# Performance work log

Measured on AMD Instinct MI355X. Metric: run time of the kernel, lower is better.

## Reference

```python
import jax, jax.numpy as jnp
import numpy as np

N_TOKENS = 100000
CUT = [0, 20000, 50000, 100000]  # cutoff_ends
D = 1024


def setup_inputs() -> dict:
    key = jax.random.key(0)
    ks = jax.random.split(key, 12)
    B, S = 2, 1024
    hidden = jax.random.normal(ks[0], (B, S, D), dtype=jnp.float32)
    target = jax.random.randint(ks[1], (B, S), 0, N_TOKENS, dtype=jnp.int64)
    s = 0.02
    # cluster 0 (shortlist) + cluster projection head
    w0 = jax.random.normal(ks[2], (20000, 1024), dtype=jnp.float32) * s
    b0 = jnp.zeros((20000,), jnp.float32)
    cluster_w = jax.random.normal(ks[3], (2, 1024), dtype=jnp.float32) * s  # n_clusters=2
    cluster_b = jnp.zeros((2,), jnp.float32)
    proj0 = jax.random.normal(ks[4], (1024, 1024), dtype=jnp.float32) * s  # d_proj x d_emb_0
    # tail cluster 1: d_emb_1 = 1024 // 4 = 256, vocab slice 20000..50000
    w1 = jax.random.normal(ks[5], (30000, 256), dtype=jnp.float32) * s
    b1 = jnp.zeros((30000,), jnp.float32)
    proj1 = jax.random.normal(ks[6], (1024, 256), dtype=jnp.float32) * s
    # tail cluster 2: d_emb_2 = 1024 // 16 = 64, vocab slice 50000..100000
    w2 = jax.random.normal(ks[7], (50000, 64), dtype=jnp.float32) * s
    b2 = jnp.zeros((50000,), jnp.float32)
    proj2 = jax.random.normal(ks[8], (1024, 64), dtype=jnp.float32) * s
    return {"hidden": hidden, "target": target,
            "w0": w0, "b0": b0, "cluster_w": cluster_w, "cluster_b": cluster_b, "proj0": proj0,
            "w1": w1, "b1": b1, "proj1": proj1,
            "w2": w2, "b2": b2, "proj2": proj2}


def reference(hidden, target, w0, b0, cluster_w, cluster_b, proj0,
              w1, b1, proj1, w2, b2, proj2):
    tgt_shape = target.shape
    h = hidden.reshape(-1, D)            # [N, d_proj]
    t = target.reshape(-1)               # [N]

    # head: shortlist logits + cluster logits, via low-rank projection
    head_w = jnp.concatenate([w0, cluster_w], axis=0)   # [20002, 1024]
    head_b = jnp.concatenate([b0, cluster_b], axis=0)
    head_logit = (h @ proj0) @ head_w.T + head_b        # [N, 20002]
    head_lp = jax.nn.log_softmax(head_logit, axis=1)

    nll = jnp.zeros(t.shape, h.dtype)

    # cluster 0 (shortlist): logprob is head_lp at the target id
    m0 = t < CUT[1]
    idx0 = jnp.clip(t, 0, CUT[1] - 1)
    lp0 = jnp.take_along_axis(head_lp, idx0[:, None], axis=1)[:, 0]
    nll = jnp.where(m0, -lp0, nll)

    # tail clusters. NOTE: faithful to original quirk head_logprob[:, -i]
    tails = [(CUT[1], CUT[2], w1, b1, proj1), (CUT[2], CUT[3], w2, b2, proj2)]
    for i, (left, right, w, b, p) in enumerate(tails, start=1):
        m = (t >= left) & (t < right)
        tail_logit = (h @ p) @ w.T + b                  # [N, right-left]
        tail_lp = jax.nn.log_softmax(tail_logit, axis=1)
        ti = jnp.clip(t - left, 0, right - left - 1)
        lp = head_lp[:, -i] + jnp.take_along_axis(tail_lp, ti[:, None], axis=1)[:, 0]
        nll = jnp.where(m, -lp, nll)

    return nll.reshape(tgt_shape)
```

## Files before the change

### kernel.cpp

```cpp
#include <hip/hip_runtime.h>
#include <cstdint>
#include <cstddef>

#define DEV static __device__ __forceinline__

typedef __attribute__((ext_vector_type(8))) short bf16x8_t;
typedef __attribute__((ext_vector_type(4))) float f32x4_t;

DEV unsigned short f2bf(float f) {
  union { float f; unsigned u; } v; v.f = f;
  unsigned r = v.u + 0x7fffu + ((v.u >> 16) & 1u);
  return (unsigned short)(r >> 16);
}

DEV void gl_lds16(const void* g, void* l) {
  __builtin_amdgcn_global_load_lds(
      (const __attribute__((address_space(1))) void*)g,
      (__attribute__((address_space(3))) void*)l,
      16, 0, 0);
}

__global__ __launch_bounds__(256)
void prep_k(const int* __restrict__ target,
            int* __restrict__ idx1, int* __restrict__ pos1,
            int* __restrict__ idx2, int* __restrict__ pos2,
            int* __restrict__ cnts,
            const float* __restrict__ p0, const float* __restrict__ p1,
            const float* __restrict__ p2, unsigned short* __restrict__ pAll,
            const float* __restrict__ s0, unsigned short* __restrict__ d0, int n0,
            const float* __restrict__ s1, unsigned short* __restrict__ d1, int n1,
            const float* __restrict__ s2, unsigned short* __restrict__ d2, int n2,
            const float* __restrict__ s3, unsigned short* __restrict__ d3, int n3,
            const float* __restrict__ s4, unsigned short* __restrict__ d4, int n4) {
  const int bid = blockIdx.x;
  const int tid = threadIdx.x;
  if (bid == 0) {
    __shared__ int c1, c2;
    if (tid == 0) { c1 = 0; c2 = 0; }
    __syncthreads();
    for (int i = tid; i < 2048; i += 256) {
      int t = target[i];
      if (t >= 20000 && t < 50000) {
        int p = atomicAdd(&c1, 1); idx1[p] = i; pos1[i] = p;
      } else if (t >= 50000) {
        int p = atomicAdd(&c2, 1); idx2[p] = i; pos2[i] = p;
      }
    }
    __syncthreads();
    if (tid == 0) { cnts[0] = c1; cnts[1] = c2; }
    return;
  }
  if (bid <= 1344) {
    __shared__ float tile[32][33];
    int b = bid - 1;
    const float* src; unsigned short* dst; int C, bx, by;
    if (b < 1024)      { src = p0; dst = pAll;               C = 1024; bx = b % 32; by = b / 32; }
    else if (b < 1280) { int q = b - 1024; src = p1; dst = pAll + 1024 * 1024; C = 256; bx = q % 8; by = q / 8; }
    else               { int q = b - 1280; src = p2; dst = pAll + 1280 * 1024; C = 64;  bx = q % 2; by = q / 2; }
    const int R = 1024;
    int tx = tid & 31, ty = tid >> 5;
    int c0 = bx * 32, r0 = by * 32;
    for (int yy = ty; yy < 32; yy += 8)
      tile[yy][tx] = src[(size_t)(r0 + yy) * C + (c0 + tx)];
    __syncthreads();
    for (int yy = ty; yy < 32; yy += 8)
      dst[(size_t)(c0 + yy) * R + (r0 + tx)] = f2bf(tile[tx][yy]);
    return;
  }
  int j = (bid - 1345) * 256 + tid;
  const float* s; unsigned short* d;
  if (j < n0) { s = s0; d = d0; }
  else { j -= n0;
    if (j < n1) { s = s1; d = d1; }
    else { j -= n1;
      if (j < n2) { s = s2; d = d2; }
      else { j -= n2;
        if (j < n3) { s = s3; d = d3; }
        else { j -= n3; if (j >= n4) return; s = s4; d = d4; }
      }
    }
  }
  float4 f = ((const float4*)s)[j];
  ushort4 o;
  o.x = f2bf(f.x); o.y = f2bf(f.y); o.z = f2bf(f.z); o.w = f2bf(f.w);
  ((ushort4*)d)[j] = o;
}

__global__ __launch_bounds__(256)
void proj_gemm_k(const unsigned short* __restrict__ A,
                 const unsigned short* __restrict__ W,
                 unsigned short* __restrict__ Cout) {
  __shared__ __align__(16) unsigned short As[128 * 32];
  __shared__ __align__(16) unsigned short Bs[128 * 32];
  const int K = 1024, V = 1344;
  const int tm = blockIdx.x, tn = blockIdx.y;
  const int m0 = tm * 128, n0 = tn * 128;
  const int tid = threadIdx.x, wid = tid >> 6, lane = tid & 63;
  const int quad = lane >> 4, l16 = lane & 15;
  const int wr = wid >> 1, wc = wid & 1;

  f32x4_t acc[4][4];
  const f32x4_t zero4 = {0.f, 0.f, 0.f, 0.f};
#pragma unroll
  for (int i = 0; i < 4; ++i)
#pragma unroll
    for (int j = 0; j < 4; ++j) acc[i][j] = zero4;

  const int srow = wid * 32 + (lane >> 2);
  const int skk  = (lane & 3) * 8;
  const unsigned short* Ap0 = A + (size_t)(m0 + srow) * K + skk;
  const unsigned short* Ap1 = A + (size_t)(m0 + srow + 16) * K + skk;
  int wrow0 = n0 + srow;      if (wrow0 > V - 1) wrow0 = V - 1;
  int wrow1 = n0 + srow + 16; if (wrow1 > V - 1) wrow1 = V - 1;
  const unsigned short* Wp0 = W + (size_t)wrow0 * K + skk;
  const unsigned short* Wp1 = W + (size_t)wrow1 * K + skk;
  unsigned short* Asw = As + wid * 1024;
  unsigned short* Bsw = Bs + wid * 1024;

  for (int k0 = 0; k0 < K; k0 += 32) {
    gl_lds16(Ap0, Asw);
    gl_lds16(Ap1, Asw + 512);
    gl_lds16(Wp0, Bsw);
    gl_lds16(Wp1, Bsw + 512);
    Ap0 += 32; Ap1 += 32; Wp0 += 32; Wp1 += 32;
    __syncthreads();
    bf16x8_t af[4], bfr[4];
#pragma unroll
    for (int i = 0; i < 4; ++i)
      af[i] = *(const bf16x8_t*)(As + (size_t)(wr * 64 + i * 16 + l16) * 32 + quad * 8);
#pragma unroll
    for (int j = 0; j < 4; ++j)
      bfr[j] = *(const bf16x8_t*)(Bs + (size_t)(wc * 64 + j * 16 + l16) * 32 + quad * 8);
#pragma unroll
    for (int i = 0; i < 4; ++i)
#pragma unroll
      for (int j = 0; j < 4; ++j)
        acc[i][j] = __builtin_amdgcn_mfma_f32_16x16x32_bf16(af[i], bfr[j], acc[i][j], 0, 0, 0);
    __syncthreads();
  }
#pragma unroll
  for (int i = 0; i < 4; ++i)
#pragma unroll
    for (int j = 0; j < 4; ++j) {
      const int n = n0 + wc * 64 + j * 16 + l16;
      if (n < V) {
#pragma unroll
        for (int r = 0; r < 4; ++r) {
          const int m = m0 + wr * 64 + i * 16 + quad * 4 + r;
          Cout[(size_t)m * V + n] = f2bf(acc[i][j][r]);
        }
      }
    }
}

__global__ __launch_bounds__(256)
void vocab_k(const unsigned short* __restrict__ Pall,
             const unsigned short* __restrict__ w0b,
             const unsigned short* __restrict__ w1b,
             const unsigned short* __restrict__ w2b,
             const float* __restrict__ b0, const float* __restrict__ cb,
             const float* __restrict__ b1, const float* __restrict__ b2,
             const int* __restrict__ idx1, const int* __restrict__ idx2,
             const int* __restrict__ cnts,
             float* __restrict__ part0, float* __restrict__ part1,
             float* __restrict__ part2,
             float* __restrict__ g0, float* __restrict__ g1,
             float* __restrict__ g2, float* __restrict__ cg,
             const int* __restrict__ target) {
  __shared__ __align__(16) unsigned short As[128 * 32];
  __shared__ __align__(16) unsigned short Bs[128 * 32];
  __shared__ float red[2][128];

  const int s = blockIdx.y;
  const unsigned short* A; const unsigned short* W; const float* bias;
  const int* rowidx = nullptr;
  float* partials; float* gathered;
  int K, V, Vmain, ntiles, tn, Meff, glo, headmode;
  if (s < 157) {
    headmode = 1; tn = s;
    A = Pall; K = 1024; W = w0b; V = 20002; Vmain = 20000; bias = b0;
    ntiles = 157; Meff = 2048; partials = part0; gathered = g0; glo = 0;
  } else if (s < 392) {
    headmode = 0; tn = s - 157;
    A = Pall + 1024; K = 256; W = w1b; V = 30000; Vmain = 30000; bias = b1;
    ntiles = 235; Meff = cnts[0]; rowidx = idx1; partials = part1;
    gathered = g1; glo = 20000;
  } else {
    headmode = 0; tn = s - 392;
    A = Pall + 1280; K = 64; W = w2b; V = 50000; Vmain = 50000; bias = b2;
    ntiles = 391; Meff = cnts[1]; rowidx = idx2; partials = part2;
    gathered = g2; glo = 50000;
  }
  const int ldA = 1344;
  const int m0 = blockIdx.x * 128, n0 = tn * 128;
  if (m0 >= Meff) return;

  const int tid = threadIdx.x, wid = tid >> 6, lane = tid & 63;
  const int quad = lane >> 4, l16 = lane & 15;
  const int wr = wid >> 1, wc = wid & 1;

  f32x4_t acc[4][4];
  const f32x4_t zero4 = {0.f, 0.f, 0.f, 0.f};
#pragma unroll
  for (int i = 0; i < 4; ++i)
#pragma unroll
    for (int j = 0; j < 4; ++j) acc[i][j] = zero4;

  const int srow = wid * 32 + (lane >> 2);
  const int skk  = (lane & 3) * 8;
  int arow0 = m0 + srow;      if (arow0 > Meff - 1) arow0 = Meff - 1;
  int arow1 = m0 + srow + 16; if (arow1 > Meff - 1) arow1 = Meff - 1;
  if (rowidx) { arow0 = rowidx[arow0]; arow1 = rowidx[arow1]; }
  const unsigned short* Ap0 = A + (size_t)arow0 * ldA + skk;
  const unsigned short* Ap1 = A + (size_t)arow1 * ldA + skk;
  int wrow0 = n0 + srow;      if (wrow0 > V - 1) wrow0 = V - 1;
  int wrow1 = n0 + srow + 16; if (wrow1 > V - 1) wrow1 = V - 1;
  const unsigned short* Wp0 = W + (size_t)wrow0 * K + skk;
  const unsigned short* Wp1 = W + (size_t)wrow1 * K + skk;
  unsigned short* Asw = As + wid * 1024;
  unsigned short* Bsw = Bs + wid * 1024;

  for (int k0 = 0; k0 < K; k0 += 32) {
    gl_lds16(Ap0, Asw);
    gl_lds16(Ap1, Asw + 512);
    gl_lds16(Wp0, Bsw);
    gl_lds16(Wp1, Bsw + 512);
    Ap0 += 32; Ap1 += 32; Wp0 += 32; Wp1 += 32;
    __syncthreads();
    bf16x8_t af[4], bfr[4];
#pragma unroll
    for (int i = 0; i < 4; ++i)
      af[i] = *(const bf16x8_t*)(As + (size_t)(wr * 64 + i * 16 + l16) * 32 + quad * 8);
#pragma unroll
    for (int j = 0; j < 4; ++j)
      bfr[j] = *(const bf16x8_t*)(Bs + (size_t)(wc * 64 + j * 16 + l16) * 32 + quad * 8);
#pragma unroll
    for (int i = 0; i < 4; ++i)
#pragma unroll
      for (int j = 0; j < 4; ++j)
        acc[i][j] = __builtin_amdgcn_mfma_f32_16x16x32_bf16(af[i], bfr[j], acc[i][j], 0, 0, 0);
    __syncthreads();
  }

  int nj[4]; float bj[4];
#pragma unroll
  for (int j = 0; j < 4; ++j) {
    nj[j] = n0 + wc * 64 + j * 16 + l16;
    bj[j] = (nj[j] < Vmain) ? bias[nj[j]]
                            : ((nj[j] < V) ? cb[nj[j] - Vmain] : 0.f);
  }
#pragma unroll
  for (int i = 0; i < 4; ++i) {
#pragma unroll
    for (int r = 0; r < 4; ++r) {
      const int row = wr * 64 + i * 16 + quad * 4 + r;
      const int gr = m0 + row;
      const int grc = (gr < Meff) ? gr : (Meff - 1);
      const int token = rowidx ? rowidx[grc] : grc;
      float v[4], sum = 0.f;
#pragma unroll
      for (int j = 0; j < 4; ++j) {
        v[j] = acc[i][j][r] + bj[j];
        if (nj[j] < V) sum += __expf(v[j]);
      }
#pragma unroll
      for (int off = 1; off < 16; off <<= 1)
        sum += __shfl_xor(sum, off, 64);
      if (l16 == 0) red[wc][row] = sum;
      const int t = target[token];
      int gi;
      if (headmode) gi = (t < 19999) ? t : 19999;
      else          gi = (t >= glo && t < glo + Vmain) ? (t - glo) : -1;
#pragma unroll
      for (int j = 0; j < 4; ++j) {
        if (nj[j] == gi) gathered[token] = v[j];
        if (headmode) {
          if (nj[j] == 20000) cg[2 * token]     = v[j];
          if (nj[j] == 20001) cg[2 * token + 1] = v[j];
        }
      }
    }
  }
  __syncthreads();
  if (tid < 128 && (m0 + tid) < Meff)
    partials[(size_t)(m0 + tid) * ntiles + tn] = red[0][tid] + red[1][tid];
}

__global__ __launch_bounds__(256)
void combine_k(const float* __restrict__ part0,
               const float* __restrict__ part1, int nt1,
               const float* __restrict__ part2, int nt2,
               const float* __restrict__ g0, const float* __restrict__ g1,
               const float* __restrict__ g2, const float* __restrict__ cg,
               const int* __restrict__ pos1, const int* __restrict__ pos2,
               const int* __restrict__ target, float* __restrict__ out) {
  const int w = threadIdx.x >> 6, lane = threadIdx.x & 63;
  const int token = blockIdx.x * 4 + w;
  const int t = target[token];

  float S = 0.f;
  for (int i = lane; i < 157; i += 64)
    S += part0[(size_t)token * 157 + i];
#pragma unroll
  for (int off = 1; off < 64; off <<= 1)
    S += __shfl_xor(S, off, 64);
  const float lse_head = __logf(S);

  float res;
  if (t < 20000) {
    res = lse_head - g0[token];
  } else {
    const float* pt; int nt; float gv, ch; int row;
    if (t < 50000) { pt = part1; nt = nt1; gv = g1[token]; ch = cg[2 * token + 1]; row = pos1[token]; }
    else           { pt = part2; nt = nt2; gv = g2[token]; ch = cg[2 * token];     row = pos2[token]; }
    float S2 = 0.f;
    for (int i = lane; i < nt; i += 64)
      S2 += pt[(size_t)row * nt + i];
#pragma unroll
    for (int off = 1; off < 64; off <<= 1)
      S2 += __shfl_xor(S2, off, 64);
    float lse_t = __logf(S2);
    res = -((ch - lse_head) + (gv - lse_t));
  }
  if (lane == 0) out[token] = res;
}

extern "C" void kernel_launch(void* const* d_in, const int* in_sizes, int n_in,
                              void* d_out, int out_size, void* d_ws, size_t ws_size,
                              hipStream_t stream) {
  (void)in_sizes; (void)n_in; (void)out_size; (void)ws_size;
  const float* hidden = (const float*)d_in[0];
  const int*   target = (const int*)d_in[1];
  const float* w0     = (const float*)d_in[2];
  const float* b0     = (const float*)d_in[3];
  const float* cw     = (const float*)d_in[4];
  const float* cb     = (const float*)d_in[5];
  const float* proj0  = (const float*)d_in[6];
  const float* w1     = (const float*)d_in[7];
  const float* b1     = (const float*)d_in[8];
  const float* proj1  = (const float*)d_in[9];
  const float* w2     = (const float*)d_in[10];
  const float* b2     = (const float*)d_in[11];
  const float* proj2  = (const float*)d_in[12];
  float* out = (float*)d_out;

  const int NT1 = 235, NT2 = 391;

  char* p = (char*)d_ws;
  auto alloc = [&](size_t bytes) {
    char* r = p; p += (bytes + 255) & ~(size_t)255; return r;
  };
  unsigned short* Hb   = (unsigned short*)alloc(2048ull * 1024 * 2);
  unsigned short* pAll = (unsigned short*)alloc(1344ull * 1024 * 2);
  unsigned short* w0b  = (unsigned short*)alloc(20002ull * 1024 * 2);
  unsigned short* w1b  = (unsigned short*)alloc(30000ull * 256 * 2);
  unsigned short* w2b  = (unsigned short*)alloc(50000ull * 64 * 2);
  unsigned short* Pall = (unsigned short*)alloc(2048ull * 1344 * 2);
  float* part0 = (float*)alloc(2048ull * 157 * 4);
  float* part1 = (float*)alloc(2048ull * NT1 * 4);
  float* part2 = (float*)alloc(2048ull * NT2 * 4);
  float* g0 = (float*)alloc(2048 * 4);
  float* g1 = (float*)alloc(2048 * 4);
  float* g2 = (float*)alloc(2048 * 4);
  float* cg = (float*)alloc(2048 * 2 * 4);
  int* idx1 = (int*)alloc(2048 * 4);
  int* pos1 = (int*)alloc(2048 * 4);
  int* idx2 = (int*)alloc(2048 * 4);
  int* pos2 = (int*)alloc(2048 * 4);
  int* cnts = (int*)alloc(2 * 4);

  const int c_h = 2048 * 1024 / 4, c_w0 = 20000 * 1024 / 4, c_cw = 2048 / 4,
            c_w1 = 30000 * 256 / 4, c_w2 = 50000 * 64 / 4;
  const int ctot = c_h + c_w0 + c_cw + c_w1 + c_w2;
  const int nb_cast = (ctot + 255) / 256;
  prep_k<<<1 + 1344 + nb_cast, 256, 0, stream>>>(
      target, idx1, pos1, idx2, pos2, cnts,
      proj0, proj1, proj2, pAll,
      hidden, Hb, c_h,
      w0, w0b, c_w0,
      cw, w0b + 20000ull * 1024, c_cw,
      w1, w1b, c_w1,
      w2, w2b, c_w2);

  proj_gemm_k<<<dim3(16, 11), 256, 0, stream>>>(Hb, pAll, Pall);

  vocab_k<<<dim3(16, 157 + NT1 + NT2), 256, 0, stream>>>(
      Pall, w0b, w1b, w2b, b0, cb, b1, b2,
      idx1, idx2, cnts, part0, part1, part2,
      g0, g1, g2, cg, target);

  combine_k<<<512, 256, 0, stream>>>(part0, part1, NT1, part2, NT2,
      g0, g1, g2, cg, pos1, pos2, target, out);
}
```

Before: 476.7 us.

## Split vocab kernel into head GEMM and weight-stationary tail stripe kernels

Replaces the single combined vocab kernel with a dedicated head kernel that uses a swizzled 1D grid for better L2 locality, plus two tail kernels. Each tail kernel block loads its 128-row weight slice into LDS once and loops over all routed token tiles, which removes repeated weight reloads and the per-block branch overhead. The cost is three serial launches instead of one. Tail blocks also now process every token tile sequentially with no load/compute overlap, and the large LDS footprint with launch bounds of one block limits occupancy.

```diff
diff --git a/kernel.cpp b/kernel.cpp
--- a/kernel.cpp
+++ b/kernel.cpp
@@ -154,46 +154,21 @@
 }
 
 __global__ __launch_bounds__(256)
-void vocab_k(const unsigned short* __restrict__ Pall,
-             const unsigned short* __restrict__ w0b,
-             const unsigned short* __restrict__ w1b,
-             const unsigned short* __restrict__ w2b,
-             const float* __restrict__ b0, const float* __restrict__ cb,
-             const float* __restrict__ b1, const float* __restrict__ b2,
-             const int* __restrict__ idx1, const int* __restrict__ idx2,
-             const int* __restrict__ cnts,
-             float* __restrict__ part0, float* __restrict__ part1,
-             float* __restrict__ part2,
-             float* __restrict__ g0, float* __restrict__ g1,
-             float* __restrict__ g2, float* __restrict__ cg,
-             const int* __restrict__ target) {
+void head_k(const unsigned short* __restrict__ Pall,
+            const unsigned short* __restrict__ w0b,
+            const float* __restrict__ b0, const float* __restrict__ cb,
+            float* __restrict__ part0, float* __restrict__ g0,
+            float* __restrict__ cg, const int* __restrict__ target) {
   __shared__ __align__(16) unsigned short As[128 * 32];
   __shared__ __align__(16) unsigned short Bs[128 * 32];
   __shared__ float red[2][128];
 
-  const int s = blockIdx.y;
-  const unsigned short* A; const unsigned short* W; const float* bias;
-  const int* rowidx = nullptr;
-  float* partials; float* gathered;
-  int K, V, Vmain, ntiles, tn, Meff, glo, headmode;
-  if (s < 157) {
-    headmode = 1; tn = s;
-    A = Pall; K = 1024; W = w0b; V = 20002; Vmain = 20000; bias = b0;
-    ntiles = 157; Meff = 2048; partials = part0; gathered = g0; glo = 0;
-  } else if (s < 392) {
-    headmode = 0; tn = s - 157;
-    A = Pall + 1024; K = 256; W = w1b; V = 30000; Vmain = 30000; bias = b1;
-    ntiles = 235; Meff = cnts[0]; rowidx = idx1; partials = part1;
-    gathered = g1; glo = 20000;
-  } else {
-    headmode = 0; tn = s - 392;
-    A = Pall + 1280; K = 64; W = w2b; V = 50000; Vmain = 50000; bias = b2;
-    ntiles = 391; Meff = cnts[1]; rowidx = idx2; partials = part2;
-    gathered = g2; glo = 50000;
-  }
-  const int ldA = 1344;
-  const int m0 = blockIdx.x * 128, n0 = tn * 128;
-  if (m0 >= Meff) return;
+  const int bid = blockIdx.x;
+  const int x = (bid >> 3) & 15;
+  const int y = ((bid >> 7) << 3) | (bid & 7);
+  if (y >= 157) return;
+  const int K = 1024, V = 20002, Vmain = 20000, ldA = 1344;
+  const int m0 = x * 128, n0 = y * 128;
 
   const int tid = threadIdx.x, wid = tid >> 6, lane = tid & 63;
   const int quad = lane >> 4, l16 = lane & 15;
@@ -208,15 +183,12 @@
 
   const int srow = wid * 32 + (lane >> 2);
   const int skk  = (lane & 3) * 8;
-  int arow0 = m0 + srow;      if (arow0 > Meff - 1) arow0 = Meff - 1;
-  int arow1 = m0 + srow + 16; if (arow1 > Meff - 1) arow1 = Meff - 1;
-  if (rowidx) { arow0 = rowidx[arow0]; arow1 = rowidx[arow1]; }
-  const unsigned short* Ap0 = A + (size_t)arow0 * ldA + skk;
-  const unsigned short* Ap1 = A + (size_t)arow1 * ldA + skk;
+  const unsigned short* Ap0 = Pall + (size_t)(m0 + srow) * ldA + skk;
+  const unsigned short* Ap1 = Pall + (size_t)(m0 + srow + 16) * ldA + skk;
   int wrow0 = n0 + srow;      if (wrow0 > V - 1) wrow0 = V - 1;
   int wrow1 = n0 + srow + 16; if (wrow1 > V - 1) wrow1 = V - 1;
-  const unsigned short* Wp0 = W + (size_t)wrow0 * K + skk;
-  const unsigned short* Wp1 = W + (size_t)wrow1 * K + skk;
+  const unsigned short* Wp0 = w0b + (size_t)wrow0 * K + skk;
+  const unsigned short* Wp1 = w0b + (size_t)wrow1 * K + skk;
   unsigned short* Asw = As + wid * 1024;
   unsigned short* Bsw = Bs + wid * 1024;
 
@@ -246,17 +218,14 @@
 #pragma unroll
   for (int j = 0; j < 4; ++j) {
     nj[j] = n0 + wc * 64 + j * 16 + l16;
-    bj[j] = (nj[j] < Vmain) ? bias[nj[j]]
-                            : ((nj[j] < V) ? cb[nj[j] - Vmain] : 0.f);
+    bj[j] = (nj[j] < Vmain) ? b0[nj[j]] : ((nj[j] < V) ? cb[nj[j] - Vmain] : 0.f);
   }
 #pragma unroll
   for (int i = 0; i < 4; ++i) {
 #pragma unroll
     for (int r = 0; r < 4; ++r) {
       const int row = wr * 64 + i * 16 + quad * 4 + r;
-      const int gr = m0 + row;
-      const int grc = (gr < Meff) ? gr : (Meff - 1);
-      const int token = rowidx ? rowidx[grc] : grc;
+      const int token = m0 + row;
       float v[4], sum = 0.f;
 #pragma unroll
       for (int j = 0; j < 4; ++j) {
@@ -268,22 +237,121 @@
         sum += __shfl_xor(sum, off, 64);
       if (l16 == 0) red[wc][row] = sum;
       const int t = target[token];
-      int gi;
-      if (headmode) gi = (t < 19999) ? t : 19999;
-      else          gi = (t >= glo && t < glo + Vmain) ? (t - glo) : -1;
+      const int gi = (t < 19999) ? t : 19999;
 #pragma unroll
       for (int j = 0; j < 4; ++j) {
-        if (nj[j] == gi) gathered[token] = v[j];
-        if (headmode) {
-          if (nj[j] == 20000) cg[2 * token]     = v[j];
-          if (nj[j] == 20001) cg[2 * token + 1] = v[j];
+        if (nj[j] == gi) g0[token] = v[j];
+        if (nj[j] == 20000) cg[2 * token]     = v[j];
+        if (nj[j] == 20001) cg[2 * token + 1] = v[j];
+      }
+    }
+  }
+  __syncthreads();
+  if (tid < 128)
+    part0[(size_t)(m0 + tid) * 157 + y] = red[0][tid] + red[1][tid];
+}
+
+template <int KT>
+__global__ __launch_bounds__(256, 1)
+void tail_stripe_k(const unsigned short* __restrict__ A, int ldA,
+                   const unsigned short* __restrict__ W,
+                   const float* __restrict__ bias, int V, int ntiles,
+                   const int* __restrict__ rowidx,
+                   const int* __restrict__ cnt_ptr,
+                   float* __restrict__ partials,
+                   float* __restrict__ gathered,
+                   const int* __restrict__ target, int glo) {
+  constexpr int NC = KT / 32;
+  __shared__ __align__(16) unsigned short Ws[NC][128 * 32];
+  __shared__ __align__(16) unsigned short As[NC][128 * 32];
+  __shared__ float red[2][128];
+
+  const int tn = blockIdx.x, n0 = tn * 128;
+  const int Meff = *cnt_ptr;
+  const int tid = threadIdx.x, wid = tid >> 6, lane = tid & 63;
+  const int quad = lane >> 4, l16 = lane & 15;
+  const int wr = wid >> 1, wc = wid & 1;
+  const int srow = wid * 32 + (lane >> 2);
+  const int skk  = (lane & 3) * 8;
+
+  int wrow0 = n0 + srow;      if (wrow0 > V - 1) wrow0 = V - 1;
+  int wrow1 = n0 + srow + 16; if (wrow1 > V - 1) wrow1 = V - 1;
+#pragma unroll
+  for (int c = 0; c < NC; ++c) {
+    gl_lds16(W + (size_t)wrow0 * KT + c * 32 + skk, Ws[c] + wid * 1024);
+    gl_lds16(W + (size_t)wrow1 * KT + c * 32 + skk, Ws[c] + wid * 1024 + 512);
+  }
+
+  int nj[4]; float bj[4];
+#pragma unroll
+  for (int j = 0; j < 4; ++j) {
+    nj[j] = n0 + wc * 64 + j * 16 + l16;
+    bj[j] = (nj[j] < V) ? bias[nj[j]] : 0.f;
+  }
+
+  const int nm = (Meff + 127) >> 7;
+  for (int m = 0; m < nm; ++m) {
+    const int m0 = m * 128;
+    int ar0 = m0 + srow;      if (ar0 > Meff - 1) ar0 = Meff - 1;
+    int ar1 = m0 + srow + 16; if (ar1 > Meff - 1) ar1 = Meff - 1;
+    ar0 = rowidx[ar0]; ar1 = rowidx[ar1];
+#pragma unroll
+    for (int c = 0; c < NC; ++c) {
+      gl_lds16(A + (size_t)ar0 * ldA + c * 32 + skk, As[c] + wid * 1024);
+      gl_lds16(A + (size_t)ar1 * ldA + c * 32 + skk, As[c] + wid * 1024 + 512);
+    }
+    __syncthreads();
+
+    f32x4_t acc[4][4];
+    const f32x4_t zero4 = {0.f, 0.f, 0.f, 0.f};
+#pragma unroll
+    for (int i = 0; i < 4; ++i)
+#pragma unroll
+      for (int j = 0; j < 4; ++j) acc[i][j] = zero4;
+#pragma unroll
+    for (int c = 0; c < NC; ++c) {
+      bf16x8_t af[4], bfr[4];
+#pragma unroll
+      for (int i = 0; i < 4; ++i)
+        af[i] = *(const bf16x8_t*)(As[c] + (size_t)(wr * 64 + i * 16 + l16) * 32 + quad * 8);
+#pragma unroll
+      for (int j = 0; j < 4; ++j)
+        bfr[j] = *(const bf16x8_t*)(Ws[c] + (size_t)(wc * 64 + j * 16 + l16) * 32 + quad * 8);
+#pragma unroll
+      for (int i = 0; i < 4; ++i)
+#pragma unroll
+        for (int j = 0; j < 4; ++j)
+          acc[i][j] = __builtin_amdgcn_mfma_f32_16x16x32_bf16(af[i], bfr[j], acc[i][j], 0, 0, 0);
+    }
+
+#pragma unroll
+    for (int i = 0; i < 4; ++i) {
+#pragma unroll
+      for (int r = 0; r < 4; ++r) {
+        const int row = wr * 64 + i * 16 + quad * 4 + r;
+        const int gr = m0 + row;
+        const int grc = (gr < Meff) ? gr : (Meff - 1);
+        const int token = rowidx[grc];
+        float v[4], sum = 0.f;
+#pragma unroll
+        for (int j = 0; j < 4; ++j) {
+          v[j] = acc[i][j][r] + bj[j];
+          if (nj[j] < V) sum += __expf(v[j]);
         }
-      }
-    }
-  }
-  __syncthreads();
-  if (tid < 128 && (m0 + tid) < Meff)
-    partials[(size_t)(m0 + tid) * ntiles + tn] = red[0][tid] + red[1][tid];
+#pragma unroll
+        for (int off = 1; off < 16; off <<= 1)
+          sum += __shfl_xor(sum, off, 64);
+        if (l16 == 0) red[wc][row] = sum;
+        const int gi = target[token] - glo;
+#pragma unroll
+        for (int j = 0; j < 4; ++j)
+          if (nj[j] == gi) gathered[token] = v[j];
+      }
+    }
+    __syncthreads();
+    if (tid < 128 && (m0 + tid) < Meff)
+      partials[(size_t)(m0 + tid) * ntiles + tn] = red[0][tid] + red[1][tid];
+  }
 }
 
 __global__ __launch_bounds__(256)
@@ -384,10 +452,14 @@
 
   proj_gemm_k<<<dim3(16, 11), 256, 0, stream>>>(Hb, pAll, Pall);
 
-  vocab_k<<<dim3(16, 157 + NT1 + NT2), 256, 0, stream>>>(
-      Pall, w0b, w1b, w2b, b0, cb, b1, b2,
-      idx1, idx2, cnts, part0, part1, part2,
-      g0, g1, g2, cg, target);
+  head_k<<<2560, 256, 0, stream>>>(Pall, w0b, b0, cb, part0, g0, cg, target);
+
+  tail_stripe_k<256><<<NT1, 256, 0, stream>>>(
+      Pall + 1024, 1344, w1b, b1, 30000, NT1, idx1, cnts + 0,
+      part1, g1, target, 20000);
+  tail_stripe_k<64><<<NT2, 256, 0, stream>>>(
+      Pall + 1280, 1344, w2b, b2, 50000, NT2, idx2, cnts + 1,
+      part2, g2, target, 50000);
 
   combine_k<<<512, 256, 0, stream>>>(part0, part1, NT1, part2, NT2,
       g0, g1, g2, cg, pos1, pos2, target, out);
```

Result: faster. 425.8 us (-10.7%).
